# Optimization experiments

Hardware: AMD Instinct MI355X
Metric: run time of the kernel (lower is better)

Reference implementation:

```python
import jax, jax.numpy as jnp
import numpy as np

D = 1024      # n_embedding
H = 16        # n_head
DH = D // H   # head_size = 64
T = 2048      # block_size / seq len
B = 2
EPS = 1e-5


def layer_norm(x, gamma, beta):
    mu = jnp.mean(x, axis=-1, keepdims=True)
    var = jnp.mean((x - mu) ** 2, axis=-1, keepdims=True)
    return (x - mu) * jax.lax.rsqrt(var + EPS) * gamma + beta


def setup_inputs() -> dict:
    key = jax.random.key(0)
    ks = jax.random.split(key, 12)
    s = 0.02
    return {
        "x": jax.random.normal(ks[0], (B, T, D), jnp.float32),
        # per-head QKV projections stacked over heads: [H, D, DH] (no bias, as in Head)
        "wq": jax.random.normal(ks[1], (H, D, DH), jnp.float32) * s,
        "wk": jax.random.normal(ks[2], (H, D, DH), jnp.float32) * s,
        "wv": jax.random.normal(ks[3], (H, D, DH), jnp.float32) * s,
        # output projection [H*DH, D] with bias
        "w_proj": jax.random.normal(ks[4], (H * DH, D), jnp.float32) * s,
        "b_proj": jnp.zeros((D,), jnp.float32),
        # feedforward: D -> 4D -> D
        "w1": jax.random.normal(ks[5], (D, 4 * D), jnp.float32) * s,
        "b1": jnp.zeros((4 * D,), jnp.float32),
        "w2": jax.random.normal(ks[6], (4 * D, D), jnp.float32) * s,
        "b2": jnp.zeros((D,), jnp.float32),
        # layer norms
        "ln1_g": jnp.ones((D,), jnp.float32),
        "ln1_b": jnp.zeros((D,), jnp.float32),
        "ln2_g": jnp.ones((D,), jnp.float32),
        "ln2_b": jnp.zeros((D,), jnp.float32),
    }


def reference(x, wq, wk, wv, w_proj, b_proj, w1, b1, w2, b2,
              ln1_g, ln1_b, ln2_g, ln2_b):
    # pre-LN attention sub-block
    xn = layer_norm(x, ln1_g, ln1_b)                      # [B,T,D]
    q = jnp.einsum('btd,hdk->bhtk', xn, wq)               # [B,H,T,DH]
    k = jnp.einsum('btd,hdk->bhtk', xn, wk)
    v = jnp.einsum('btd,hdk->bhtk', xn, wv)
    scale = DH ** -0.5
    scores = jnp.einsum('bhtk,bhsk->bhts', q, k) * scale  # [B,H,T,T]
    causal = jnp.tril(jnp.ones((T, T), bool))
    scores = jnp.where(causal, scores, -jnp.inf)
    attn = jax.nn.softmax(scores, axis=-1)
    out = jnp.einsum('bhts,bhsk->bhtk', attn, v)          # [B,H,T,DH]
    out = out.transpose(0, 2, 1, 3).reshape(B, T, H * DH)  # concat heads
    x = x + out @ w_proj + b_proj                          # residual 1
    # pre-LN feedforward sub-block
    xn2 = layer_norm(x, ln2_g, ln2_b)
    h = jax.nn.relu(xn2 @ w1 + b1)
    x = x + h @ w2 + b2                                    # residual 2
    return x
```

## Files before the change

### kernel.cpp

```cpp
#include <hip/hip_runtime.h>
#include <hip/hip_bf16.h>
#include <math.h>


#define D_MODEL 1024
#define NH 16
#define DHEAD 64
#define SEQ 2048
#define NTOK 4096

typedef __bf16 bf16x8 __attribute__((ext_vector_type(8)));
typedef float f32x4 __attribute__((ext_vector_type(4)));
typedef float f32x16 __attribute__((ext_vector_type(16)));
typedef unsigned short u16x8 __attribute__((ext_vector_type(8)));

__device__ __forceinline__ unsigned short f2b(float f) {
  unsigned u = __builtin_bit_cast(unsigned, f);
  u = u + 0x7fffu + ((u >> 16) & 1u);
  return (unsigned short)(u >> 16);
}

__device__ __forceinline__ bf16x8 ld_bf16x8(const unsigned short* p) {
  u16x8 u = *(const u16x8*)p;
  return __builtin_bit_cast(bf16x8, u);
}

__device__ __forceinline__ void async16(void* lds, const void* g) {
  __builtin_amdgcn_global_load_lds(
      (const __attribute__((address_space(1))) unsigned int*)g,
      (__attribute__((address_space(3))) unsigned int*)lds, 16, 0, 0);
}

__device__ __forceinline__ bf16x8 ds_read16(const void* p) {
  bf16x8 r;
  unsigned a = (unsigned)(size_t)(const __attribute__((address_space(3))) void*)p;
  asm volatile("ds_read_b128 %0, %1" : "=v"(r) : "v"(a));
  return r;
}
__device__ __forceinline__ void ds_write32(void* p, unsigned v) {
  unsigned a = (unsigned)(size_t)(__attribute__((address_space(3))) void*)p;
  asm volatile("ds_write_b32 %0, %1" :: "v"(a), "v"(v));
}
__device__ __forceinline__ unsigned cvt_pk_bf16(float lo, float hi) {
  unsigned d;
  asm("v_cvt_pk_bf16_f32 %0, %1, %2" : "=v"(d) : "v"(lo), "v"(hi));
  return d;
}
#define WAIT_LGKM0_FENCE() do { \
  asm volatile("s_waitcnt lgkmcnt(0)" ::: "memory"); \
  __builtin_amdgcn_sched_barrier(0); } while (0)


__global__ __launch_bounds__(256) void repack_qkv(
    const float* __restrict__ wq, const float* __restrict__ wk,
    const float* __restrict__ wv, unsigned short* __restrict__ outT) {
  __shared__ float tile[64][65];
  int t = blockIdx.x;
  int sel = t >> 8;
  int h = (t >> 4) & 15;
  int rt = t & 15;
  const float* in = (sel == 0 ? wq : sel == 1 ? wk : wv) + (size_t)h * D_MODEL * DHEAD;
  int d0 = rt * 64;
  for (int i = 0; i < 16; i++) {
    int idx = i * 256 + threadIdx.x;
    int r = idx >> 6, c = idx & 63;
    tile[r][c] = in[(size_t)(d0 + r) * DHEAD + c];
  }
  __syncthreads();
  unsigned short* ob = outT + (size_t)(sel * 1024 + h * 64) * D_MODEL + d0;
  for (int i = 0; i < 16; i++) {
    int idx = i * 256 + threadIdx.x;
    int c = idx >> 6, r = idx & 63;
    ob[(size_t)c * D_MODEL + r] = f2b(tile[r][c]);
  }
}

__global__ __launch_bounds__(256) void transpose_to_bf16(
    const float* __restrict__ in, unsigned short* __restrict__ out, int R, int C) {
  __shared__ float tile[64][65];
  int r0 = blockIdx.x * 64, c0 = blockIdx.y * 64;
  for (int i = 0; i < 16; i++) {
    int idx = i * 256 + threadIdx.x;
    int r = idx >> 6, c = idx & 63;
    tile[r][c] = in[(size_t)(r0 + r) * C + c0 + c];
  }
  __syncthreads();
  for (int i = 0; i < 16; i++) {
    int idx = i * 256 + threadIdx.x;
    int c = idx >> 6, r = idx & 63;
    out[(size_t)(c0 + c) * R + r0 + r] = f2b(tile[r][c]);
  }
}

__global__ __launch_bounds__(256) void layernorm_bf16(
    const float* __restrict__ x, const float* __restrict__ g,
    const float* __restrict__ bta, unsigned short* __restrict__ out) {
  int row = blockIdx.x;
  int tid = threadIdx.x;
  const float4* xr = (const float4*)(x + (size_t)row * D_MODEL);
  float4 v = xr[tid];
  float s = v.x + v.y + v.z + v.w;
  float s2 = v.x * v.x + v.y * v.y + v.z * v.z + v.w * v.w;
  for (int m = 1; m < 64; m <<= 1) {
    s += __shfl_xor(s, m);
    s2 += __shfl_xor(s2, m);
  }
  __shared__ float ps[4], ps2[4];
  int wid = tid >> 6;
  if ((tid & 63) == 0) { ps[wid] = s; ps2[wid] = s2; }
  __syncthreads();
  float S = ps[0] + ps[1] + ps[2] + ps[3];
  float S2 = ps2[0] + ps2[1] + ps2[2] + ps2[3];
  float mu = S * (1.f / D_MODEL);
  float var = S2 * (1.f / D_MODEL) - mu * mu;
  float inv = rsqrtf(var + 1e-5f);
  float4 gv = ((const float4*)g)[tid];
  float4 bv = ((const float4*)bta)[tid];
  ushort4 o;
  o.x = f2b((v.x - mu) * inv * gv.x + bv.x);
  o.y = f2b((v.y - mu) * inv * gv.y + bv.y);
  o.z = f2b((v.z - mu) * inv * gv.z + bv.z);
  o.w = f2b((v.w - mu) * inv * gv.w + bv.w);
  ((ushort4*)(out + (size_t)row * D_MODEL))[tid] = o;
}

template <int MODE>
__global__ __launch_bounds__(256, 2) void gemm_p4(
    const unsigned short* __restrict__ A, const unsigned short* __restrict__ BT,
    int M, int N, int K,
    const float* __restrict__ bias, const float* __restrict__ resid,
    float* __restrict__ outF,
    unsigned short* __restrict__ outQ, unsigned short* __restrict__ outK,
    unsigned short* __restrict__ outV) {
  __shared__ alignas(16) unsigned short lsA[2][128 * 64];
  __shared__ alignas(16) unsigned short lsB[2][128 * 64];
  const int tid = threadIdx.x;
  const int wid = tid >> 6, lane = tid & 63;
  const int lr = lane & 15, lg = lane >> 4;
  const int row0 = blockIdx.x * 128, col0 = blockIdx.y * 128;
  const int wr = (wid >> 1) * 64, wc = (wid & 1) * 64;
  f32x4 acc[4][4] = {};
  const int nk = K >> 6;

  auto STAGE = [&](int bi, int kt) {
    const int k0 = kt << 6;
#pragma unroll
    for (int i = 0; i < 4; i++) {
      int sidx = i * 256 + tid;
      int r = sidx >> 3, s = sidx & 7;
      int ss = s ^ (r & 7);
      async16((char*)lsA[bi] + (i * 256 + wid * 64) * 16,
              A + (size_t)(row0 + r) * K + k0 + ss * 8);
      async16((char*)lsB[bi] + (i * 256 + wid * 64) * 16,
              BT + (size_t)(col0 + r) * K + k0 + ss * 8);
    }
  };

  STAGE(0, 0);
  for (int kt = 0; kt < nk; ++kt) {
    const int cur = kt & 1;
    if (kt + 1 < nk) {
      STAGE(cur ^ 1, kt + 1);
      asm volatile("s_waitcnt vmcnt(8)" ::: "memory");
    } else {
      asm volatile("s_waitcnt vmcnt(0)" ::: "memory");
    }
    __builtin_amdgcn_s_barrier();
    __builtin_amdgcn_sched_barrier(0);
#pragma unroll
    for (int kk = 0; kk < 2; ++kk) {
      bf16x8 af[4], bfr[4];
#pragma unroll
      for (int m = 0; m < 4; m++) {
        int r = wr + m * 16 + lr;
        int sw = (kk * 4 + lg) ^ (r & 7);
        af[m] = ds_read16((const char*)lsA[cur] + r * 128 + sw * 16);
      }
#pragma unroll
      for (int n = 0; n < 4; n++) {
        int r = wc + n * 16 + lr;
        int sw = (kk * 4 + lg) ^ (r & 7);
        bfr[n] = ds_read16((const char*)lsB[cur] + r * 128 + sw * 16);
      }
      WAIT_LGKM0_FENCE();
      __builtin_amdgcn_s_setprio(1);
#pragma unroll
      for (int m = 0; m < 4; m++)
#pragma unroll
        for (int n = 0; n < 4; n++)
          acc[m][n] = __builtin_amdgcn_mfma_f32_16x16x32_bf16(af[m], bfr[n], acc[m][n], 0, 0, 0);
      __builtin_amdgcn_s_setprio(0);
    }
    __builtin_amdgcn_sched_barrier(0);
    __builtin_amdgcn_s_barrier();
  }
#pragma unroll
  for (int m = 0; m < 4; m++) {
#pragma unroll
    for (int n = 0; n < 4; n++) {
#pragma unroll
      for (int r2 = 0; r2 < 4; r2++) {
        int row = row0 + wr + m * 16 + lg * 4 + r2;
        int col = col0 + wc + n * 16 + lr;
        float v = acc[m][n][r2];
        if constexpr (MODE == 0) {
          v += bias[col] + resid[(size_t)row * N + col];
          outF[(size_t)row * N + col] = v;
        } else {
          int sel = col >> 10, jj = col & 1023, h = jj >> 6, dh = jj & 63;
          int b = row >> 11, t = row & 2047;
          size_t bh = (size_t)(b * NH + h);
          if (sel == 0)      outQ[(bh * SEQ + t) * DHEAD + dh] = f2b(v);
          else if (sel == 1) outK[(bh * SEQ + t) * DHEAD + dh] = f2b(v);
          else               outV[(bh * DHEAD + dh) * SEQ + t] = f2b(v);
        }
      }
    }
  }
}

template <int TAG>
__global__ __launch_bounds__(512, 1) void gemm_bt8(
    const unsigned short* __restrict__ A, const unsigned short* __restrict__ BT,
    int M, int N, int K,
    const float* __restrict__ bias, const float* __restrict__ resid,
    float* __restrict__ outF) {
  __shared__ alignas(16) unsigned short lsA[3][128 * 64];
  __shared__ alignas(16) unsigned short lsB[3][128 * 64];
  const int tid = threadIdx.x;
  const int wid = tid >> 6, lane = tid & 63;
  const int lr = lane & 15, lg = lane >> 4;
  const int row0 = blockIdx.x * 128, col0 = blockIdx.y * 128;
  const int wr = (wid >> 2) * 64, wc = (wid & 3) * 32;
  f32x4 acc[4][2] = {};
  const int nk = K >> 6;

  auto STAGE = [&](int bi, int kt) {
    const int k0 = kt << 6;
#pragma unroll
    for (int i = 0; i < 2; i++) {
      int sidx = i * 512 + tid;
      int r = sidx >> 3, s = sidx & 7;
      int ss = s ^ (r & 7);
      async16((char*)lsA[bi] + (i * 512 + wid * 64) * 16,
              A + (size_t)(row0 + r) * K + k0 + ss * 8);
      async16((char*)lsB[bi] + (i * 512 + wid * 64) * 16,
              BT + (size_t)(col0 + r) * K + k0 + ss * 8);
    }
  };

  STAGE(0, 0);
  if (nk > 1) STAGE(1, 1);
  for (int kt = 0; kt < nk; ++kt) {
    const int cur = kt % 3;
    if (kt + 2 < nk) {
      STAGE((kt + 2) % 3, kt + 2);
      asm volatile("s_waitcnt vmcnt(8)" ::: "memory");
    } else if (kt + 1 < nk) {
      asm volatile("s_waitcnt vmcnt(4)" ::: "memory");
    } else {
      asm volatile("s_waitcnt vmcnt(0)" ::: "memory");
    }
    __builtin_amdgcn_s_barrier();
    __builtin_amdgcn_sched_barrier(0);
#pragma unroll
    for (int kk = 0; kk < 2; ++kk) {
      bf16x8 af[4], bfr[2];
#pragma unroll
      for (int m = 0; m < 4; m++) {
        int r = wr + m * 16 + lr;
        int sw = (kk * 4 + lg) ^ (r & 7);
        af[m] = ds_read16((const char*)lsA[cur] + r * 128 + sw * 16);
      }
#pragma unroll
      for (int n = 0; n < 2; n++) {
        int r = wc + n * 16 + lr;
        int sw = (kk * 4 + lg) ^ (r & 7);
        bfr[n] = ds_read16((const char*)lsB[cur] + r * 128 + sw * 16);
      }
      WAIT_LGKM0_FENCE();
      __builtin_amdgcn_s_setprio(1);
#pragma unroll
      for (int m = 0; m < 4; m++)
#pragma unroll
        for (int n = 0; n < 2; n++)
          acc[m][n] = __builtin_amdgcn_mfma_f32_16x16x32_bf16(af[m], bfr[n], acc[m][n], 0, 0, 0);
      __builtin_amdgcn_s_setprio(0);
    }
    __builtin_amdgcn_sched_barrier(0);
    __builtin_amdgcn_s_barrier();
  }
#pragma unroll
  for (int m = 0; m < 4; m++) {
#pragma unroll
    for (int n = 0; n < 2; n++) {
#pragma unroll
      for (int r2 = 0; r2 < 4; r2++) {
        int row = row0 + wr + m * 16 + lg * 4 + r2;
        int col = col0 + wc + n * 16 + lr;
        float v = acc[m][n][r2] + bias[col] + resid[(size_t)row * N + col];
        outF[(size_t)row * N + col] = v;
      }
    }
  }
}

__global__ __launch_bounds__(512, 2) void gemm256_bt(
    const unsigned short* __restrict__ A, const unsigned short* __restrict__ BT,
    int M, int N, int K, int ntn,
    const float* __restrict__ bias, unsigned short* __restrict__ outB) {
  __shared__ alignas(16) unsigned short ls[2][2][2][256 * 32];
  const int tid = threadIdx.x;
  const int wid = tid >> 6, lane = tid & 63;
  const int lr = lane & 15, lg = lane >> 4;
  const int nwg = gridDim.x;
  const int wg = (blockIdx.x & 7) * (nwg >> 3) + (blockIdx.x >> 3);
  const int row0 = (wg / ntn) * 256, col0 = (wg % ntn) * 256;
  const int mbase = (wid >> 2) * 128;
  const int nbase = (wid & 3) * 64;

  f32x4 acc[8][4] = {};

  auto STAGE = [&](int buf, int kh, int ab, int kt) {
    const unsigned short* src = ab ? (BT + (size_t)col0 * K) : (A + (size_t)row0 * K);
    const int kbase = kt * 64 + kh * 32;
    unsigned short* dst0 = &ls[buf][kh][ab][0];
#pragma unroll
    for (int c = 0; c < 2; c++) {
      int s = c * 512 + tid;
      int row = s >> 2, c2 = s & 3;
      int ss = c2 ^ ((row >> 1) & 3);
      async16(dst0 + (size_t)(c * 512 + wid * 64) * 8,
              src + (size_t)row * K + kbase + ss * 8);
    }
  };
  auto LDA = [&](bf16x8* a, int buf, int kk, int mh) {
#pragma unroll
    for (int i = 0; i < 4; i++) {
      int mrow = mbase + (mh * 4 + i) * 16 + lr;
      int ch = lg ^ ((mrow >> 1) & 3);
      a[i] = ds_read16(&ls[buf][kk][0][mrow * 32 + ch * 8]);
    }
  };
  auto LDB = [&](bf16x8* b, int buf, int kk) {
#pragma unroll
    for (int i = 0; i < 4; i++) {
      int brow = nbase + i * 16 + lr;
      int ch = lg ^ ((brow >> 1) & 3);
      b[i] = ds_read16(&ls[buf][kk][1][brow * 32 + ch * 8]);
    }
  };

  const int nk = K >> 6;
  STAGE(0, 0, 0, 0); STAGE(0, 0, 1, 0); STAGE(0, 1, 0, 0); STAGE(0, 1, 1, 0);
  asm volatile("s_waitcnt vmcnt(4)" ::: "memory");
  __builtin_amdgcn_s_barrier();

  for (int t = 0; t < nk; ++t) {
    const int cur = t & 1, nxt = cur ^ 1;
    const bool haveNext = (t + 1 < nk);
    bf16x8 a[4], b[4];
    LDA(a, cur, 0, 0); LDB(b, cur, 0);
    if (haveNext) STAGE(nxt, 0, 0, t + 1);
    __builtin_amdgcn_s_barrier();
    WAIT_LGKM0_FENCE();
    __builtin_amdgcn_s_setprio(1);
#pragma unroll
    for (int i = 0; i < 4; i++)
#pragma unroll
      for (int j = 0; j < 4; j++)
        acc[i][j] = __builtin_amdgcn_mfma_f32_16x16x32_bf16(a[i], b[j], acc[i][j], 0, 0, 0);
    __builtin_amdgcn_s_setprio(0);
    __builtin_amdgcn_s_barrier();
    LDA(a, cur, 0, 1);
    if (haveNext) {
      STAGE(nxt, 0, 1, t + 1);
      asm volatile("s_waitcnt vmcnt(4)" ::: "memory");
    } else {
      asm volatile("s_waitcnt vmcnt(0)" ::: "memory");
    }
    __builtin_amdgcn_s_barrier();
    WAIT_LGKM0_FENCE();
    __builtin_amdgcn_s_setprio(1);
#pragma unroll
    for (int i = 0; i < 4; i++)
#pragma unroll
      for (int j = 0; j < 4; j++)
        acc[4 + i][j] = __builtin_amdgcn_mfma_f32_16x16x32_bf16(a[i], b[j], acc[4 + i][j], 0, 0, 0);
    __builtin_amdgcn_s_setprio(0);
    __builtin_amdgcn_s_barrier();
    LDA(a, cur, 1, 0); LDB(b, cur, 1);
    if (haveNext) STAGE(nxt, 1, 0, t + 1);
    __builtin_amdgcn_s_barrier();
    WAIT_LGKM0_FENCE();
    __builtin_amdgcn_s_setprio(1);
#pragma unroll
    for (int i = 0; i < 4; i++)
#pragma unroll
      for (int j = 0; j < 4; j++)
        acc[i][j] = __builtin_amdgcn_mfma_f32_16x16x32_bf16(a[i], b[j], acc[i][j], 0, 0, 0);
    __builtin_amdgcn_s_setprio(0);
    __builtin_amdgcn_s_barrier();
    LDA(a, cur, 1, 1);
    if (haveNext) {
      STAGE(nxt, 1, 1, t + 1);
      asm volatile("s_waitcnt vmcnt(4)" ::: "memory");
    }
    __builtin_amdgcn_s_barrier();
    WAIT_LGKM0_FENCE();
    __builtin_amdgcn_s_setprio(1);
#pragma unroll
    for (int i = 0; i < 4; i++)
#pragma unroll
      for (int j = 0; j < 4; j++)
        acc[4 + i][j] = __builtin_amdgcn_mfma_f32_16x16x32_bf16(a[i], b[j], acc[4 + i][j], 0, 0, 0);
    __builtin_amdgcn_s_setprio(0);
    __builtin_amdgcn_s_barrier();
  }
#pragma unroll
  for (int mi = 0; mi < 8; mi++) {
#pragma unroll
    for (int ni = 0; ni < 4; ni++) {
#pragma unroll
      for (int r2 = 0; r2 < 4; r2++) {
        int row = row0 + mbase + mi * 16 + lg * 4 + r2;
        int col = col0 + nbase + ni * 16 + lr;
        float v = acc[mi][ni][r2] + bias[col];
        outB[(size_t)row * N + col] = f2b(fmaxf(v, 0.f));
      }
    }
  }
}

__global__ __launch_bounds__(256, 2) void attn_fwd(
    const unsigned short* __restrict__ Q, const unsigned short* __restrict__ K,
    const unsigned short* __restrict__ VT, unsigned short* __restrict__ O) {
  __shared__ alignas(16) unsigned short Kl[2][8192];
  __shared__ alignas(16) unsigned short Vl[2][8192];
  const int tid = threadIdx.x, wid = tid >> 6, lane = tid & 63;
  const int l31 = lane & 31, h = lane >> 5;
  const int sid = (int)(blockIdx.x & 7) * 64 + (int)(blockIdx.x >> 3);
  const int bh = sid >> 4, qt = 15 - (sid & 15);
  const unsigned short* Qb = Q + (size_t)bh * SEQ * DHEAD;
  const unsigned short* Kb = K + (size_t)bh * SEQ * DHEAD;
  const unsigned short* Vb = VT + (size_t)bh * DHEAD * SEQ;
  const int q0w = qt * 128 + wid * 32;
  bf16x8 qf[4];
#pragma unroll
  for (int dk = 0; dk < 4; dk++)
    qf[dk] = ld_bf16x8(Qb + (size_t)(q0w + l31) * DHEAD + dk * 16 + h * 8);
  f32x16 o0 = {}, o1 = {};
  float psum = 0.f;
  const float cs = 0.18033688011112042f;
  const int nsteps = qt + 1;

  auto STAGE = [&](unsigned short* Kd, unsigned short* Vd, int s0) {
#pragma unroll
    for (int c = 0; c < 4; c++) {
      int s = c * 256 + tid;
      int row = s >> 3, sl = s & 7;
      int ss = sl ^ (row & 7);
      async16((char*)Kd + (c * 256 + wid * 64) * 16,
              Kb + (size_t)(s0 + row) * DHEAD + ss * 8);
    }
#pragma unroll
    for (int c = 0; c < 4; c++) {
      int s = c * 256 + tid;
      int row = s >> 4, sl = s & 15;
      int ss = sl ^ (row & 7);
      async16((char*)Vd + (c * 256 + wid * 64) * 16,
              Vb + (size_t)row * SEQ + s0 + ss * 8);
    }
  };

  STAGE(Kl[0], Vl[0], 0);
  for (int t = 0; t < nsteps; ++t) {
    if (t + 1 < nsteps) {
      STAGE(Kl[(t + 1) & 1], Vl[(t + 1) & 1], (t + 1) * 128);
      asm volatile("s_waitcnt vmcnt(8)" ::: "memory");
    } else {
      asm volatile("s_waitcnt vmcnt(0)" ::: "memory");
    }
    __builtin_amdgcn_s_barrier();
    __builtin_amdgcn_sched_barrier(0);
    const unsigned short* Kc = Kl[t & 1];
    const unsigned short* Vc = Vl[t & 1];
    const int s0 = t * 128;
#pragma unroll
    for (int g = 0; g < 4; g++) {
      const int s0g = s0 + 32 * g;
      if (s0g <= q0w) {
        const bool needMask = (s0g == q0w);
        bf16x8 kf[4], vf[4];
        {
          int krow = 32 * g + l31;
          int ksw = krow & 7;
#pragma unroll
          for (int dk = 0; dk < 4; dk++) {
            int ch = (2 * dk + h) ^ ksw;
            kf[dk] = ds_read16((const char*)Kc + krow * 128 + ch * 16);
          }
#pragma unroll
          for (int dg = 0; dg < 2; dg++) {
            int vrow = 32 * dg + l31;
            int vsw = vrow & 7;
#pragma unroll
            for (int c = 0; c < 2; c++) {
              int kk = 2 * g + c;
              int ch = (2 * kk + h) ^ vsw;
              vf[dg * 2 + c] = ds_read16((const char*)Vc + vrow * 256 + ch * 16);
            }
          }
        }
        WAIT_LGKM0_FENCE();
        f32x16 st = {};
#pragma unroll
        for (int dk = 0; dk < 4; dk++)
          st = __builtin_amdgcn_mfma_f32_32x32x16_bf16(kf[dk], qf[dk], st, 0, 0, 0);
        float p[16];
#pragma unroll
        for (int reg = 0; reg < 16; reg++) {
          float xx = st[reg] * cs;
          if (needMask) {
            int kg = s0g + (reg & 3) + 8 * (reg >> 2) + 4 * h;
            if (kg > q0w + l31) xx = -INFINITY;
          }
          float e = __builtin_amdgcn_exp2f(xx);
          p[reg] = e;
          psum += e;
        }
        unsigned w[8];
#pragma unroll
        for (int s = 0; s < 4; s++) {
          w[s * 2 + 0] = cvt_pk_bf16(p[s * 4 + 0], p[s * 4 + 1]);
          w[s * 2 + 1] = cvt_pk_bf16(p[s * 4 + 2], p[s * 4 + 3]);
        }
#pragma unroll
        for (int c = 0; c < 2; c++) {
          unsigned a0 = w[(2 * c) * 2 + 0], b0 = w[(2 * c + 1) * 2 + 0];
          unsigned a1 = w[(2 * c) * 2 + 1], b1 = w[(2 * c + 1) * 2 + 1];
          asm volatile("v_permlane32_swap_b32 %0, %1" : "+v"(a0), "+v"(b0));
          asm volatile("v_permlane32_swap_b32 %0, %1" : "+v"(a1), "+v"(b1));
          uint4 pw = {a0, a1, b0, b1};
          bf16x8 pf = __builtin_bit_cast(bf16x8, pw);
          o0 = __builtin_amdgcn_mfma_f32_32x32x16_bf16(vf[0 * 2 + c], pf, o0, 0, 0, 0);
          o1 = __builtin_amdgcn_mfma_f32_32x32x16_bf16(vf[1 * 2 + c], pf, o1, 0, 0, 0);
        }
      }
    }
    __builtin_amdgcn_sched_barrier(0);
    __builtin_amdgcn_s_barrier();
  }
  psum += __shfl_xor(psum, 32);
  float inv = 1.f / psum;
  unsigned short* slice = (unsigned short*)Kl + wid * 2048;
#pragma unroll
  for (int dg = 0; dg < 2; dg++) {
#pragma unroll
    for (int s = 0; s < 4; s++) {
#pragma unroll
      for (int m = 0; m < 2; m++) {
        float va = (dg ? o1[s * 4 + 2 * m] : o0[s * 4 + 2 * m]) * inv;
        float vb = (dg ? o1[s * 4 + 2 * m + 1] : o0[s * 4 + 2 * m + 1]) * inv;
        unsigned wv = cvt_pk_bf16(va, vb);
        int d = 32 * dg + 8 * s + 4 * h + 2 * m;
        ds_write32(&slice[l31 * 64 + d], wv);
      }
    }
  }
  WAIT_LGKM0_FENCE();
  bf16x8 ov[4];
#pragma unroll
  for (int pss = 0; pss < 4; pss++) {
    int qrow = pss * 8 + (lane >> 3);
    int d0 = (lane & 7) * 8;
    ov[pss] = ds_read16(&slice[qrow * 64 + d0]);
  }
  WAIT_LGKM0_FENCE();
  const int b = bh >> 4, head = bh & 15;
#pragma unroll
  for (int pss = 0; pss < 4; pss++) {
    int qrow = pss * 8 + (lane >> 3);
    int d0 = (lane & 7) * 8;
    *(bf16x8*)(O + ((size_t)b * SEQ + q0w + qrow) * D_MODEL + head * DHEAD + d0) = ov[pss];
  }
}


extern "C" void kernel_launch(void* const* d_in, const int* in_sizes, int n_in,
                              void* d_out, int out_size, void* d_ws, size_t ws_size,
                              hipStream_t stream) {
  const float* x = (const float*)d_in[0];
  const float* wq = (const float*)d_in[1];
  const float* wk = (const float*)d_in[2];
  const float* wv = (const float*)d_in[3];
  const float* w_proj = (const float*)d_in[4];
  const float* b_proj = (const float*)d_in[5];
  const float* w1 = (const float*)d_in[6];
  const float* b1 = (const float*)d_in[7];
  const float* w2 = (const float*)d_in[8];
  const float* b2 = (const float*)d_in[9];
  const float* ln1g = (const float*)d_in[10];
  const float* ln1b = (const float*)d_in[11];
  const float* ln2g = (const float*)d_in[12];
  const float* ln2b = (const float*)d_in[13];

  char* ws = (char*)d_ws;
  const size_t MB = 1024ull * 1024ull;
  unsigned short* xn = (unsigned short*)(ws + 0);
  unsigned short* Qb = (unsigned short*)(ws + 8 * MB);
  unsigned short* Kb = (unsigned short*)(ws + 16 * MB);
  unsigned short* VTb = (unsigned short*)(ws + 24 * MB);
  unsigned short* aout = (unsigned short*)(ws + 32 * MB);
  unsigned short* hbuf = (unsigned short*)(ws + 40 * MB);
  unsigned short* WqkvT = (unsigned short*)(ws + 72 * MB);
  unsigned short* wprojT = (unsigned short*)(ws + 78 * MB);
  unsigned short* w1T = (unsigned short*)(ws + 80 * MB);
  unsigned short* w2T = (unsigned short*)(ws + 88 * MB);
  float* x1 = (float*)d_out;

  repack_qkv<<<dim3(768), 256, 0, stream>>>(wq, wk, wv, WqkvT);
  transpose_to_bf16<<<dim3(16, 16), 256, 0, stream>>>(w_proj, wprojT, 1024, 1024);
  transpose_to_bf16<<<dim3(16, 64), 256, 0, stream>>>(w1, w1T, 1024, 4096);
  transpose_to_bf16<<<dim3(64, 16), 256, 0, stream>>>(w2, w2T, 4096, 1024);

  layernorm_bf16<<<NTOK, 256, 0, stream>>>(x, ln1g, ln1b, xn);
  gemm_p4<2><<<dim3(32, 24), 256, 0, stream>>>(xn, WqkvT, NTOK, 3072, 1024,
      nullptr, nullptr, nullptr, Qb, Kb, VTb);
  attn_fwd<<<dim3(512), 256, 0, stream>>>(Qb, Kb, VTb, aout);
  gemm_bt8<0><<<dim3(32, 8), 512, 0, stream>>>(aout, wprojT, NTOK, 1024, 1024,
      b_proj, x, x1);
  layernorm_bf16<<<NTOK, 256, 0, stream>>>(x1, ln2g, ln2b, xn);
  gemm256_bt<<<dim3(256), 512, 0, stream>>>(xn, w1T, NTOK, 4096, 1024, 16,
      b1, hbuf);
  gemm_bt8<1><<<dim3(32, 8), 512, 0, stream>>>(hbuf, w2T, NTOK, 1024, 4096,
      b2, x1, (float*)d_out);
}
```

Measured before the change: 234.7 us.

## Software-pipeline LDS reads across key groups in attention with dual accumulators

Restructures the attention inner loop so the LDS reads for the next 32-key group are issued before computing the current group, with a partial lgkmcnt wait. Alternating register sets and two accumulator pairs break the serial MFMA dependency chain, and the row sum is split across four partial sums. This aims to hide LDS latency and MFMA accumulate latency. The cost is higher VGPR pressure, which could hurt occupancy at two blocks per CU.

```diff
diff --git a/kernel.cpp b/kernel.cpp
--- a/kernel.cpp
+++ b/kernel.cpp
@@ -48,6 +48,9 @@
 }
 #define WAIT_LGKM0_FENCE() do { \
   asm volatile("s_waitcnt lgkmcnt(0)" ::: "memory"); \
+  __builtin_amdgcn_sched_barrier(0); } while (0)
+#define WAIT_LGKM8_FENCE() do { \
+  asm volatile("s_waitcnt lgkmcnt(8)" ::: "memory"); \
   __builtin_amdgcn_sched_barrier(0); } while (0)
 
 
@@ -432,6 +435,66 @@
   }
 }
 
+
+#define ATTN_READS(KF, VF, G) do {                                          \
+  int krow_ = 32 * (G) + l31;                                               \
+  int ksw_ = krow_ & 7;                                                     \
+  _Pragma("unroll")                                                         \
+  for (int dk_ = 0; dk_ < 4; dk_++) {                                       \
+    int ch_ = (2 * dk_ + h) ^ ksw_;                                         \
+    KF[dk_] = ds_read16((const char*)Kc + krow_ * 128 + ch_ * 16);          \
+  }                                                                         \
+  _Pragma("unroll")                                                         \
+  for (int dg_ = 0; dg_ < 2; dg_++) {                                       \
+    int vrow_ = 32 * dg_ + l31;                                             \
+    int vsw_ = vrow_ & 7;                                                   \
+    _Pragma("unroll")                                                       \
+    for (int c_ = 0; c_ < 2; c_++) {                                        \
+      int kk_ = 2 * (G) + c_;                                               \
+      int ch_ = (2 * kk_ + h) ^ vsw_;                                       \
+      VF[dg_ * 2 + c_] = ds_read16((const char*)Vc + vrow_ * 256 + ch_ * 16); \
+    }                                                                       \
+  }                                                                         \
+} while (0)
+
+#define ATTN_COMPUTE(KF, VF, G, OA, OB) do {                                \
+  const int s0g_ = s0 + 32 * (G);                                           \
+  const bool needMask_ = (s0g_ == q0w);                                     \
+  f32x16 st_ = {};                                                          \
+  _Pragma("unroll")                                                         \
+  for (int dk_ = 0; dk_ < 4; dk_++)                                         \
+    st_ = __builtin_amdgcn_mfma_f32_32x32x16_bf16(KF[dk_], qf[dk_], st_, 0, 0, 0); \
+  float p_[16];                                                             \
+  _Pragma("unroll")                                                         \
+  for (int reg_ = 0; reg_ < 16; reg_++) {                                   \
+    float xx_ = st_[reg_] * cs;                                             \
+    if (needMask_) {                                                        \
+      int kg_ = s0g_ + (reg_ & 3) + 8 * (reg_ >> 2) + 4 * h;                \
+      if (kg_ > q0w + l31) xx_ = -INFINITY;                                 \
+    }                                                                       \
+    float e_ = __builtin_amdgcn_exp2f(xx_);                                 \
+    p_[reg_] = e_;                                                          \
+    psum4[reg_ & 3] += e_;                                                  \
+  }                                                                         \
+  unsigned w_[8];                                                           \
+  _Pragma("unroll")                                                         \
+  for (int s_ = 0; s_ < 4; s_++) {                                          \
+    w_[s_ * 2 + 0] = cvt_pk_bf16(p_[s_ * 4 + 0], p_[s_ * 4 + 1]);           \
+    w_[s_ * 2 + 1] = cvt_pk_bf16(p_[s_ * 4 + 2], p_[s_ * 4 + 3]);           \
+  }                                                                         \
+  _Pragma("unroll")                                                         \
+  for (int c_ = 0; c_ < 2; c_++) {                                          \
+    unsigned a0_ = w_[(2 * c_) * 2 + 0], b0_ = w_[(2 * c_ + 1) * 2 + 0];    \
+    unsigned a1_ = w_[(2 * c_) * 2 + 1], b1_ = w_[(2 * c_ + 1) * 2 + 1];    \
+    asm volatile("v_permlane32_swap_b32 %0, %1" : "+v"(a0_), "+v"(b0_));    \
+    asm volatile("v_permlane32_swap_b32 %0, %1" : "+v"(a1_), "+v"(b1_));    \
+    uint4 pw_ = {a0_, a1_, b0_, b1_};                                       \
+    bf16x8 pf_ = __builtin_bit_cast(bf16x8, pw_);                           \
+    OA = __builtin_amdgcn_mfma_f32_32x32x16_bf16(VF[0 * 2 + c_], pf_, OA, 0, 0, 0); \
+    OB = __builtin_amdgcn_mfma_f32_32x32x16_bf16(VF[1 * 2 + c_], pf_, OB, 0, 0, 0); \
+  }                                                                         \
+} while (0)
+
 __global__ __launch_bounds__(256, 2) void attn_fwd(
     const unsigned short* __restrict__ Q, const unsigned short* __restrict__ K,
     const unsigned short* __restrict__ VT, unsigned short* __restrict__ O) {
@@ -449,8 +512,8 @@
 #pragma unroll
   for (int dk = 0; dk < 4; dk++)
     qf[dk] = ld_bf16x8(Qb + (size_t)(q0w + l31) * DHEAD + dk * 16 + h * 8);
-  f32x16 o0 = {}, o1 = {};
-  float psum = 0.f;
+  f32x16 o0a = {}, o1a = {}, o0b = {}, o1b = {};
+  float psum4[4] = {0.f, 0.f, 0.f, 0.f};
   const float cs = 0.18033688011112042f;
   const int nsteps = qt + 1;
 
@@ -486,71 +549,33 @@
     const unsigned short* Kc = Kl[t & 1];
     const unsigned short* Vc = Vl[t & 1];
     const int s0 = t * 128;
-#pragma unroll
-    for (int g = 0; g < 4; g++) {
-      const int s0g = s0 + 32 * g;
-      if (s0g <= q0w) {
-        const bool needMask = (s0g == q0w);
-        bf16x8 kf[4], vf[4];
-        {
-          int krow = 32 * g + l31;
-          int ksw = krow & 7;
-#pragma unroll
-          for (int dk = 0; dk < 4; dk++) {
-            int ch = (2 * dk + h) ^ ksw;
-            kf[dk] = ds_read16((const char*)Kc + krow * 128 + ch * 16);
-          }
-#pragma unroll
-          for (int dg = 0; dg < 2; dg++) {
-            int vrow = 32 * dg + l31;
-            int vsw = vrow & 7;
-#pragma unroll
-            for (int c = 0; c < 2; c++) {
-              int kk = 2 * g + c;
-              int ch = (2 * kk + h) ^ vsw;
-              vf[dg * 2 + c] = ds_read16((const char*)Vc + vrow * 256 + ch * 16);
-            }
+    const int ng = (s0 <= q0w) ? ((q0w - s0) >> 5) >= 3 ? 4 : (((q0w - s0) >> 5) + 1) : 0;
+    if (ng > 0) {
+      bf16x8 kfA[4], vfA[4], kfB[4], vfB[4];
+      ATTN_READS(kfA, vfA, 0);
+      if (ng > 1) { ATTN_READS(kfB, vfB, 1); WAIT_LGKM8_FENCE(); }
+      else        { WAIT_LGKM0_FENCE(); }
+      ATTN_COMPUTE(kfA, vfA, 0, o0a, o1a);
+      if (ng > 1) {
+        if (ng > 2) { ATTN_READS(kfA, vfA, 2); WAIT_LGKM8_FENCE(); }
+        else        { WAIT_LGKM0_FENCE(); }
+        ATTN_COMPUTE(kfB, vfB, 1, o0b, o1b);
+        if (ng > 2) {
+          if (ng > 3) { ATTN_READS(kfB, vfB, 3); WAIT_LGKM8_FENCE(); }
+          else        { WAIT_LGKM0_FENCE(); }
+          ATTN_COMPUTE(kfA, vfA, 2, o0a, o1a);
+          if (ng > 3) {
+            WAIT_LGKM0_FENCE();
+            ATTN_COMPUTE(kfB, vfB, 3, o0b, o1b);
           }
         }
-        WAIT_LGKM0_FENCE();
-        f32x16 st = {};
-#pragma unroll
-        for (int dk = 0; dk < 4; dk++)
-          st = __builtin_amdgcn_mfma_f32_32x32x16_bf16(kf[dk], qf[dk], st, 0, 0, 0);
-        float p[16];
-#pragma unroll
-        for (int reg = 0; reg < 16; reg++) {
-          float xx = st[reg] * cs;
-          if (needMask) {
-            int kg = s0g + (reg & 3) + 8 * (reg >> 2) + 4 * h;
-            if (kg > q0w + l31) xx = -INFINITY;
-          }
-          float e = __builtin_amdgcn_exp2f(xx);
-          p[reg] = e;
-          psum += e;
-        }
-        unsigned w[8];
-#pragma unroll
-        for (int s = 0; s < 4; s++) {
-          w[s * 2 + 0] = cvt_pk_bf16(p[s * 4 + 0], p[s * 4 + 1]);
-          w[s * 2 + 1] = cvt_pk_bf16(p[s * 4 + 2], p[s * 4 + 3]);
-        }
-#pragma unroll
-        for (int c = 0; c < 2; c++) {
-          unsigned a0 = w[(2 * c) * 2 + 0], b0 = w[(2 * c + 1) * 2 + 0];
-          unsigned a1 = w[(2 * c) * 2 + 1], b1 = w[(2 * c + 1) * 2 + 1];
-          asm volatile("v_permlane32_swap_b32 %0, %1" : "+v"(a0), "+v"(b0));
-          asm volatile("v_permlane32_swap_b32 %0, %1" : "+v"(a1), "+v"(b1));
-          uint4 pw = {a0, a1, b0, b1};
-          bf16x8 pf = __builtin_bit_cast(bf16x8, pw);
-          o0 = __builtin_amdgcn_mfma_f32_32x32x16_bf16(vf[0 * 2 + c], pf, o0, 0, 0, 0);
-          o1 = __builtin_amdgcn_mfma_f32_32x32x16_bf16(vf[1 * 2 + c], pf, o1, 0, 0, 0);
-        }
       }
     }
     __builtin_amdgcn_sched_barrier(0);
     __builtin_amdgcn_s_barrier();
   }
+  f32x16 o0 = o0a + o0b, o1 = o1a + o1b;
+  float psum = (psum4[0] + psum4[1]) + (psum4[2] + psum4[3]);
   psum += __shfl_xor(psum, 32);
   float inv = 1.f / psum;
   unsigned short* slice = (unsigned short*)Kl + wid * 2048;
```

Result: no change. 233.5 us (-0.5%).
